# Performance work log

Measured on AMD Instinct MI355X. Metric: run time of the kernel, lower is better.

## Reference

```python
import jax, jax.numpy as jnp
import numpy as np

THRESH = 0.01
PADDING = (1, 1)   # (pad_w, pad_h) as in torch code: ZeroPad2d((p0,p0,p1,p1))
STRIDE = (1, 1)


def setup_inputs() -> dict:
    key = jax.random.key(0)
    k1, k2, k3 = jax.random.split(key, 3)
    x = jax.random.normal(k1, (4, 32, 128, 128), dtype=jnp.float32)
    weight = jax.random.normal(k2, (32, 32, 3, 3), dtype=jnp.float32) * 0.05
    bias = jax.random.normal(k3, (32,), dtype=jnp.float32) * 0.05
    return {"x": x, "weight": weight, "bias": bias}


def reference(x, weight, bias):
    p0, p1 = PADDING
    s0, s1 = STRIDE
    B, C, H, W = x.shape
    O, _, kr, kc = weight.shape

    # ZeroPad2d((p0, p0, p1, p1)): left/right by p0, top/bottom by p1
    xp = jnp.pad(x, ((0, 0), (0, 0), (p1, p1), (p0, p0)))
    xr, xc = H + 2 * p1, W + 2 * p0
    N = xr * xc

    # Flatten spatial dims and FFT along length-N axis; threshold-prune coeffs
    x_fft = jnp.fft.fft(xp.reshape(B, C, N))                    # (B, C, N) complex
    x_fft = jnp.where(jnp.abs(x_fft.real) < THRESH, 0.0, x_fft)

    # Pad kernel to (xr, xc) bottom/right, flatten, reverse along last dim.
    # (torch.flip([0,1]) then flip([0,1,2]) nets out to a flip on dim 2 only.)
    W_pad = jnp.pad(weight, ((0, 0), (0, 0), (0, xr - kr), (0, xc - kc)))
    W_fft = jnp.fft.fft(W_pad.reshape(O, C, N)[:, :, ::-1])     # (O, C, N) complex

    # Batched circular convolution: (B,1,C,N) * (1,O,C,N)
    y = jnp.fft.ifft(x_fft[:, None, :, :] * W_fft[None, :, :, :]).real  # (B,O,C,N)

    # torch.roll(y, 1) with no dim rolls the FLATTENED (C*N) tensor per (b,o)
    y = jnp.roll(y.reshape(B, O, C * N), 1, axis=-1).reshape(B, O, C, xr, xc)
    y = y.sum(axis=2)                                           # (B, O, xr, xc)

    ans_row = -(-(xr - kr + 1) // s0)  # ceil division
    ans_col = -(-(xc - kc + 1) // s1)
    y = y[:, :, ::s0, ::s1][:, :, :ans_row, :ans_col]
    return y + bias[None, :, None, None]
```

## Files before the change

kernel.cpp:

```cpp
#include <hip/hip_runtime.h>


typedef __attribute__((ext_vector_type(8))) short short8;
typedef __attribute__((ext_vector_type(4))) float f32x4;
typedef __attribute__((ext_vector_type(4))) unsigned int u32x4;

__device__ __forceinline__ unsigned short f2bf(float f) {
    unsigned int u = __builtin_bit_cast(unsigned int, f);
    u += 0x7FFFu + ((u >> 16) & 1u);
    return (unsigned short)(u >> 16);
}

__global__ __launch_bounds__(256)
void transpose_x(const float* __restrict__ x, unsigned short* __restrict__ xt) {
    const int pg = blockIdx.x * 256 + threadIdx.x;
    const int b  = pg >> 14;
    const int px = pg & 16383;
    const float* xp = x + (size_t)b * 32 * 16384 + px;
    unsigned int u[16];
    #pragma unroll
    for (int cp = 0; cp < 16; ++cp) {
        const float f0 = xp[(size_t)(2 * cp)     * 16384];
        const float f1 = xp[(size_t)(2 * cp + 1) * 16384];
        u[cp] = (unsigned)f2bf(f0) | ((unsigned)f2bf(f1) << 16);
    }
    u32x4* dst = (u32x4*)(xt + (size_t)pg * 32);
    #pragma unroll
    for (int q = 0; q < 4; ++q) {
        u32x4 v;
        v[0] = u[4*q]; v[1] = u[4*q+1]; v[2] = u[4*q+2]; v[3] = u[4*q+3];
        dst[q] = v;
    }
}

__global__ void transpose_w(const float* __restrict__ w, unsigned short* __restrict__ wt) {
    const int idx = blockIdx.x * 256 + threadIdx.x;
    if (idx < 9216) {
        const int t = idx >> 10;
        const int o = (idx >> 5) & 31;
        const int c = idx & 31;
        wt[idx] = f2bf(w[(o * 32 + c) * 9 + t]);
    }
}

__global__ __launch_bounds__(256, 4)
void conv_mfma(const unsigned short* __restrict__ xt,
               const unsigned short* __restrict__ wt,
               const float* __restrict__ bias,
               float* __restrict__ out) {
    const int tid  = threadIdx.x;
    const int wave = tid >> 6;
    const int lane = tid & 63;
    const int lm   = lane & 15;
    const int quad = lane >> 4;
    const int q8   = quad * 8;

    const int g  = blockIdx.x * 4 + wave;
    const int b  = g >> 10;
    const int i  = (g >> 3) & 127;
    const int j0 = (g & 7) * 16;
    const int j  = j0 + lm;

    u32x4 af[9][2];
    #pragma unroll
    for (int t = 0; t < 9; ++t)
        #pragma unroll
        for (int mt = 0; mt < 2; ++mt)
            af[t][mt] = *(const u32x4*)(wt + ((t * 32 + mt * 16 + lm) * 32 + q8));

    f32x4 acc0 = {0.f, 0.f, 0.f, 0.f};
    f32x4 acc1 = {0.f, 0.f, 0.f, 0.f};
    const unsigned short* xb = xt + (size_t)b * 16384 * 32;

    #pragma unroll
    for (int t = 0; t < 9; ++t) {
        const int r  = t / 3, s = t - 3 * r;
        const int si = i + r - 1;
        const int sj = j + s - 1;
        const bool ok = ((unsigned)si < 128u) && ((unsigned)sj < 128u);
        const int ci = min(max(si, 0), 127);
        const int cj = min(max(sj, 0), 127);
        u32x4 bv = *(const u32x4*)(xb + ((size_t)(ci * 128 + cj) * 32 + q8));
        const unsigned msk = ok ? 0xFFFFFFFFu : 0u;
        bv &= msk;
        const short8 bs = __builtin_bit_cast(short8, bv);
        acc0 = __builtin_amdgcn_mfma_f32_16x16x32_bf16(
                   __builtin_bit_cast(short8, af[t][0]), bs, acc0, 0, 0, 0);
        acc1 = __builtin_amdgcn_mfma_f32_16x16x32_bf16(
                   __builtin_bit_cast(short8, af[t][1]), bs, acc1, 0, 0, 0);
    }

    const size_t pixbase = (size_t)i * 128 + j0 + lm;
    #pragma unroll
    for (int reg = 0; reg < 4; ++reg) {
        const int o0 = quad * 4 + reg;
        const int o1 = 16 + o0;
        out[((size_t)(b * 32 + o0) << 14) + pixbase] = acc0[reg] + bias[o0];
        out[((size_t)(b * 32 + o1) << 14) + pixbase] = acc1[reg] + bias[o1];
    }
}

extern "C" void kernel_launch(void* const* d_in, const int* in_sizes, int n_in,
                              void* d_out, int out_size, void* d_ws, size_t ws_size,
                              hipStream_t stream) {
    const float* x    = (const float*)d_in[0];
    const float* w    = (const float*)d_in[1];
    const float* bias = (const float*)d_in[2];
    float* out = (float*)d_out;

    unsigned short* xt = (unsigned short*)d_ws;
    unsigned short* wt = (unsigned short*)((char*)d_ws + (4 << 20));

    hipLaunchKernelGGL(transpose_x, dim3(256), dim3(256), 0, stream, x, xt);
    hipLaunchKernelGGL(transpose_w, dim3(36),  dim3(256), 0, stream, w, wt);
    hipLaunchKernelGGL(conv_mfma,   dim3(1024), dim3(256), 0, stream,
                       xt, wt, bias, out);
}
```

Baseline: 77.82 us.

## Fuse input/weight bf16 conversion into conv kernel with LDS staging

Replaces the three-kernel pipeline (input transpose, weight transpose, MFMA conv) with one fused kernel. Each block loads a 3-row by 66-column halo of the input straight from the NCHW fp32 tensor, converts it to packed bf16 in shared memory, and also converts all weights into shared memory. MFMA operands are then read from LDS instead of a global workspace. This removes two launches and the workspace write and read-back. In exchange, every block redundantly converts the full weight tensor, and halo rows are loaded up to three times across blocks.

```diff
diff --git a/kernel.cpp b/kernel.cpp
--- a/kernel.cpp
+++ b/kernel.cpp
@@ -11,78 +11,75 @@
     return (unsigned short)(u >> 16);
 }
 
-__global__ __launch_bounds__(256)
-void transpose_x(const float* __restrict__ x, unsigned short* __restrict__ xt) {
-    const int pg = blockIdx.x * 256 + threadIdx.x;
-    const int b  = pg >> 14;
-    const int px = pg & 16383;
-    const float* xp = x + (size_t)b * 32 * 16384 + px;
-    unsigned int u[16];
+__global__ __launch_bounds__(256, 4)
+void conv_fused(const float* __restrict__ x, const float* __restrict__ w,
+                const float* __restrict__ bias, float* __restrict__ out) {
+    const int tid  = threadIdx.x;
+    const int blk  = blockIdx.x;
+    const int b    = blk >> 8;
+    const int i    = (blk >> 1) & 127;
+    const int half = blk & 1;
+    const int c0   = half * 64;
+
+    __shared__ __align__(16) unsigned int   xls[3 * 66 * 16];
+    __shared__ __align__(16) unsigned short wls[9 * 32 * 32];
+
     #pragma unroll
-    for (int cp = 0; cp < 16; ++cp) {
-        const float f0 = xp[(size_t)(2 * cp)     * 16384];
-        const float f1 = xp[(size_t)(2 * cp + 1) * 16384];
-        u[cp] = (unsigned)f2bf(f0) | ((unsigned)f2bf(f1) << 16);
-    }
-    u32x4* dst = (u32x4*)(xt + (size_t)pg * 32);
-    #pragma unroll
-    for (int q = 0; q < 4; ++q) {
-        u32x4 v;
-        v[0] = u[4*q]; v[1] = u[4*q+1]; v[2] = u[4*q+2]; v[3] = u[4*q+3];
-        dst[q] = v;
-    }
-}
-
-__global__ void transpose_w(const float* __restrict__ w, unsigned short* __restrict__ wt) {
-    const int idx = blockIdx.x * 256 + threadIdx.x;
-    if (idx < 9216) {
+    for (int k = 0; k < 36; ++k) {
+        const int idx = tid + 256 * k;
         const int t = idx >> 10;
         const int o = (idx >> 5) & 31;
         const int c = idx & 31;
-        wt[idx] = f2bf(w[(o * 32 + c) * 9 + t]);
+        wls[idx] = f2bf(w[(o * 32 + c) * 9 + t]);
     }
-}
 
-__global__ __launch_bounds__(256, 4)
-void conv_mfma(const unsigned short* __restrict__ xt,
-               const unsigned short* __restrict__ wt,
-               const float* __restrict__ bias,
-               float* __restrict__ out) {
-    const int tid  = threadIdx.x;
+    const float* xb = x + ((size_t)b << 19);
+    const int p  = tid & 15;
+    const int l0 = tid >> 4;
+    #pragma unroll
+    for (int r = 0; r < 3; ++r) {
+        const int gi  = i - 1 + r;
+        const bool rok = (unsigned)gi < 128u;
+        const int gic = min(max(gi, 0), 127);
+        #pragma unroll
+        for (int pass = 0; pass < 5; ++pass) {
+            const int l = l0 + 16 * pass;
+            if (l < 66) {
+                const int gj  = c0 - 1 + l;
+                const bool ok = rok && ((unsigned)gj < 128u);
+                const int gjc = min(max(gj, 0), 127);
+                const size_t base = (size_t)gic * 128 + gjc;
+                float f0 = xb[((size_t)(2 * p)     << 14) + base];
+                float f1 = xb[((size_t)(2 * p + 1) << 14) + base];
+                if (!ok) { f0 = 0.f; f1 = 0.f; }
+                xls[(r * 66 + l) * 16 + p] =
+                    (unsigned)f2bf(f0) | ((unsigned)f2bf(f1) << 16);
+            }
+        }
+    }
+    __syncthreads();
+
     const int wave = tid >> 6;
     const int lane = tid & 63;
     const int lm   = lane & 15;
     const int quad = lane >> 4;
     const int q8   = quad * 8;
 
-    const int g  = blockIdx.x * 4 + wave;
-    const int b  = g >> 10;
-    const int i  = (g >> 3) & 127;
-    const int j0 = (g & 7) * 16;
-    const int j  = j0 + lm;
-
     u32x4 af[9][2];
     #pragma unroll
     for (int t = 0; t < 9; ++t)
         #pragma unroll
         for (int mt = 0; mt < 2; ++mt)
-            af[t][mt] = *(const u32x4*)(wt + ((t * 32 + mt * 16 + lm) * 32 + q8));
+            af[t][mt] = *(const u32x4*)(wls + ((t * 32 + mt * 16 + lm) * 32 + q8));
 
     f32x4 acc0 = {0.f, 0.f, 0.f, 0.f};
     f32x4 acc1 = {0.f, 0.f, 0.f, 0.f};
-    const unsigned short* xb = xt + (size_t)b * 16384 * 32;
 
     #pragma unroll
     for (int t = 0; t < 9; ++t) {
-        const int r  = t / 3, s = t - 3 * r;
-        const int si = i + r - 1;
-        const int sj = j + s - 1;
-        const bool ok = ((unsigned)si < 128u) && ((unsigned)sj < 128u);
-        const int ci = min(max(si, 0), 127);
-        const int cj = min(max(sj, 0), 127);
-        u32x4 bv = *(const u32x4*)(xb + ((size_t)(ci * 128 + cj) * 32 + q8));
-        const unsigned msk = ok ? 0xFFFFFFFFu : 0u;
-        bv &= msk;
+        const int r = t / 3, s = t - 3 * r;
+        const int l = wave * 16 + lm + s;
+        const u32x4 bv = *(const u32x4*)(xls + ((r * 66 + l) * 16 + quad * 4));
         const short8 bs = __builtin_bit_cast(short8, bv);
         acc0 = __builtin_amdgcn_mfma_f32_16x16x32_bf16(
                    __builtin_bit_cast(short8, af[t][0]), bs, acc0, 0, 0, 0);
@@ -90,6 +87,7 @@
                    __builtin_bit_cast(short8, af[t][1]), bs, acc1, 0, 0, 0);
     }
 
+    const int j0 = c0 + wave * 16;
     const size_t pixbase = (size_t)i * 128 + j0 + lm;
     #pragma unroll
     for (int reg = 0; reg < 4; ++reg) {
@@ -107,12 +105,6 @@
     const float* w    = (const float*)d_in[1];
     const float* bias = (const float*)d_in[2];
     float* out = (float*)d_out;
-
-    unsigned short* xt = (unsigned short*)d_ws;
-    unsigned short* wt = (unsigned short*)((char*)d_ws + (4 << 20));
-
-    hipLaunchKernelGGL(transpose_x, dim3(256), dim3(256), 0, stream, x, xt);
-    hipLaunchKernelGGL(transpose_w, dim3(36),  dim3(256), 0, stream, w, wt);
-    hipLaunchKernelGGL(conv_mfma,   dim3(1024), dim3(256), 0, stream,
-                       xt, wt, bias, out);
+    hipLaunchKernelGGL(conv_fused, dim3(1024), dim3(256), 0, stream,
+                       x, w, bias, out);
 }
```

New measurement: 80.71 us. +3.7%, slower.
